# Optimization experiments

Measured on AMD Instinct MI355X. Metric: run time of the kernel, lower is better.

The kernel has to match this reference:

```python
import jax, jax.numpy as jnp
import numpy as np

V = 32000   # vocab_size
H = 512     # hidden_size
B = 16      # batch
T = 128     # target_len
S = 64      # encoder seq len
L = 1       # num_layers
BOS = 1     # vocab.bos_idx


def setup_inputs() -> dict:
    key = jax.random.key(0)
    ks = jax.random.split(key, 11)
    s = 0.02  # init scale
    return {
        "encoder_outputs": jax.random.normal(ks[0], (B, S, H), jnp.float32),
        "h0": jax.random.normal(ks[1], (L, B, H), jnp.float32) * 0.1,
        "c0": jax.random.normal(ks[2], (L, B, H), jnp.float32) * 0.1,
        "target_tensor": jax.random.randint(ks[3], (B, T), 0, V, dtype=jnp.int32).astype(jnp.int64),
        "emb": jax.random.normal(ks[4], (V, H), jnp.float32) * s,
        "W_ih": jax.random.normal(ks[5], (4 * H, H), jnp.float32) * s,
        "W_hh": jax.random.normal(ks[6], (4 * H, H), jnp.float32) * s,
        "b_ih": jnp.zeros((4 * H,), jnp.float32),
        "b_hh": jnp.zeros((4 * H,), jnp.float32),
        "W_out": jax.random.normal(ks[7], (V, H), jnp.float32) * s,
        "b_out": jnp.zeros((V,), jnp.float32),
    }


def reference(encoder_outputs, h0, c0, target_tensor, emb, W_ih, W_hh, b_ih, b_hh, W_out, b_out):
    # Teacher-forced input sequence: [BOS, target[:, :-1]]  -> [B, T]
    bsz = encoder_outputs.shape[0]
    bos = jnp.full((bsz, 1), BOS, dtype=target_tensor.dtype)
    toks = jnp.concatenate([bos, target_tensor[:, :-1]], axis=1)  # [B, T]

    h, c = h0[0], c0[0]  # num_layers == 1 -> [B, H]

    def step(carry, tok):
        h, c = carry
        x = jax.nn.relu(emb[tok])                               # embed + ReLU  [B, H]
        g = x @ W_ih.T + b_ih + h @ W_hh.T + b_hh               # [B, 4H], torch gate order i,f,g,o
        i, f, gg, o = jnp.split(g, 4, axis=-1)
        c2 = jax.nn.sigmoid(f) * c + jax.nn.sigmoid(i) * jnp.tanh(gg)
        h2 = jax.nn.sigmoid(o) * jnp.tanh(c2)
        logits = h2 @ W_out.T + b_out                           # [B, V]
        return (h2, c2), logits

    (hf, cf), logits = jax.lax.scan(step, (h, c), toks.T)       # scan over time
    decoder_outputs = logits.transpose(1, 0, 2)                 # [B, T, V]
    return decoder_outputs, hf[None], cf[None]
```

## Files before the change

### kernel.cpp

```cpp
#include <hip/hip_runtime.h>
#include <hip/hip_bf16.h>
#include <cstdint>


#define V_ 32000
#define H_ 512
#define B_ 16
#define T_ 128

typedef __attribute__((ext_vector_type(8))) short s16x8;
typedef __attribute__((ext_vector_type(4))) float f32x4;

typedef unsigned int __attribute__((address_space(1))) as1_u32;
typedef unsigned int __attribute__((address_space(3))) as3_u32;

__device__ __forceinline__ void async_cp16(const void* g, void* l) {
  __builtin_amdgcn_global_load_lds((const as1_u32*)g, (as3_u32*)l, 16, 0, 0);
}

__device__ __forceinline__ short f2bf(float f) {
  union { float f; unsigned u; } v; v.f = f;
  unsigned r = v.u + 0x7fffu + ((v.u >> 16) & 1u);
  return (short)(r >> 16);
}

__global__ void cvt_bf16(const float* __restrict__ in, short* __restrict__ out, int n4) {
  int i = blockIdx.x * blockDim.x + threadIdx.x;
  if (i >= n4) return;
  float4 v = ((const float4*)in)[i];
  short4 o;
  o.x = f2bf(v.x); o.y = f2bf(v.y); o.z = f2bf(v.z); o.w = f2bf(v.w);
  ((short4*)out)[i] = o;
}

__global__ void gather_embed(const float* __restrict__ emb, const int* __restrict__ tgt,
                             short* __restrict__ X, int* __restrict__ flags) {
  int m = blockIdx.x;
  int b = m >> 7, t = m & 127;
  int tok = (t == 0) ? 1 : tgt[b * T_ + t - 1];
  int k = threadIdx.x * 4;
  float4 v = *(const float4*)&emb[(size_t)tok * H_ + k];
  short4 o;
  o.x = f2bf(fmaxf(v.x, 0.f)); o.y = f2bf(fmaxf(v.y, 0.f));
  o.z = f2bf(fmaxf(v.z, 0.f)); o.w = f2bf(fmaxf(v.w, 0.f));
  *(short4*)&X[(size_t)m * H_ + k] = o;
  if (m == 0) flags[threadIdx.x] = 0;
}

__global__ __launch_bounds__(256, 2) void gemm_bt(
    const short* __restrict__ A, const short* __restrict__ B,
    const float* __restrict__ bias0, const float* __restrict__ bias1,
    float* __restrict__ out, int M, int N, int K, int ldo)
{
  __shared__ short As[1024 * 8];
  __shared__ short Bs[1024 * 8];
  const int tid = threadIdx.x;
  const int wave = tid >> 6, lane = tid & 63;
  const int row0 = blockIdx.y * 128, col0 = blockIdx.x * 128;
  const int m_in = lane & 15, quad = lane >> 4;
  const int wm = (wave >> 1) * 64, wn = (wave & 1) * 64;
  f32x4 acc[4][4] = {};
  for (int kt = 0; kt < K; kt += 64) {
    for (int i = 0; i < 4; ++i) {
      int s = (i * 4 + wave) * 64 + lane;
      int r = s >> 3, cs = s & 7, cd = cs ^ (r & 7);
      async_cp16(A + ((size_t)(row0 + r) * K + kt + cd * 8), &As[s * 8]);
      async_cp16(B + ((size_t)(col0 + r) * K + kt + cd * 8), &Bs[s * 8]);
    }
    __syncthreads();
    for (int kk = 0; kk < 2; ++kk) {
      s16x8 af[4], bfr[4];
      int c = kk * 4 + quad;
      for (int i = 0; i < 4; ++i) {
        int ra = wm + i * 16 + m_in;
        af[i] = *(const s16x8*)&As[(ra * 8 + (c ^ (ra & 7))) * 8];
        int rb = wn + i * 16 + m_in;
        bfr[i] = *(const s16x8*)&Bs[(rb * 8 + (c ^ (rb & 7))) * 8];
      }
      for (int i = 0; i < 4; ++i)
        for (int j = 0; j < 4; ++j)
          acc[i][j] = __builtin_amdgcn_mfma_f32_16x16x32_bf16(af[i], bfr[j], acc[i][j], 0, 0, 0);
    }
    __syncthreads();
  }
  for (int j = 0; j < 4; ++j) {
    int n = col0 + wn + j * 16 + m_in;
    float bs = bias0[n] + (bias1 ? bias1[n] : 0.f);
    for (int i = 0; i < 4; ++i) {
      int mrow = row0 + wm + i * 16 + quad * 4;
      f32x4 a = acc[i][j];
      for (int p = 0; p < 4; ++p)
        out[(size_t)(mrow + p) * ldo + n] = a[p] + bs;
    }
  }
}

__global__ __launch_bounds__(512, 1) void lstm_rec(
    const float* __restrict__ G0,
    const short* __restrict__ Whh,
    const float* __restrict__ h0, const float* __restrict__ c0,
    short* __restrict__ Hs,
    int* flags,
    float* __restrict__ hcf)
{
  __shared__ short Wl[8192 * 8];
  __shared__ short hl[1024 * 8];
  __shared__ float gl[128 * 17];

  const int S = blockIdx.x;
  const int tid = threadIdx.x, wave = tid >> 6, lane = tid & 63;
  const int nin = lane & 15, quad = lane >> 4;

  for (int i = tid; i < 8192; i += 512) {
    int r = i >> 6, cs = i & 63, cd = cs ^ (r & 7);
    int u = (r >> 5) * 512 + S * 32 + (r & 31);
    *(int4*)&Wl[i * 8] = *(const int4*)&Whh[(size_t)u * H_ + cd * 8];
  }
  const int batch = tid >> 5, hid = tid & 31;
  float c_reg = c0[batch * H_ + S * 32 + hid];
  __syncthreads();

  for (int tt = 0; tt < T_; ++tt) {
    if (tt > 0) {
      if (tid == 0) {
        while (__hip_atomic_load(&flags[tt - 1], __ATOMIC_RELAXED, __HIP_MEMORY_SCOPE_AGENT) < 16) {}
        __threadfence();
      }
      __syncthreads();
    }
    for (int i = tid; i < 1024; i += 512) {
      int m = i >> 6, cs = i & 63, cd = cs ^ (m & 7);
      if (tt == 0) {
        const float* hp = &h0[m * H_ + cd * 8];
        float4 v0 = *(const float4*)hp, v1 = *(const float4*)(hp + 4);
        s16x8 o;
        o[0] = f2bf(v0.x); o[1] = f2bf(v0.y); o[2] = f2bf(v0.z); o[3] = f2bf(v0.w);
        o[4] = f2bf(v1.x); o[5] = f2bf(v1.y); o[6] = f2bf(v1.z); o[7] = f2bf(v1.w);
        *(s16x8*)&hl[i * 8] = o;
      } else {
        *(int4*)&hl[i * 8] = *(const int4*)&Hs[((size_t)m * T_ + tt - 1) * H_ + cd * 8];
      }
    }
    __syncthreads();
    f32x4 acc = {};
    {
      int r = wave * 16 + nin;
      for (int ks = 0; ks < 16; ++ks) {
        int c = ks * 4 + quad;
        s16x8 af = *(const s16x8*)&hl[(nin * 64 + (c ^ (nin & 7))) * 8];
        s16x8 bf = *(const s16x8*)&Wl[(r * 64 + (c ^ (r & 7))) * 8];
        acc = __builtin_amdgcn_mfma_f32_16x16x32_bf16(af, bf, acc, 0, 0, 0);
      }
      int u = wave * 16 + nin;
      for (int p = 0; p < 4; ++p)
        gl[u * 17 + quad * 4 + p] = acc[p];
    }
    __syncthreads();
    {
      size_t gbase = ((size_t)batch * T_ + tt) * 2048 + S * 32 + hid;
      float xi = G0[gbase         ] + gl[(0 * 32 + hid) * 17 + batch];
      float xf = G0[gbase +  512  ] + gl[(1 * 32 + hid) * 17 + batch];
      float xg = G0[gbase + 1024  ] + gl[(2 * 32 + hid) * 17 + batch];
      float xo = G0[gbase + 1536  ] + gl[(3 * 32 + hid) * 17 + batch];
      float si = 1.f / (1.f + __expf(-xi));
      float sf = 1.f / (1.f + __expf(-xf));
      float so = 1.f / (1.f + __expf(-xo));
      c_reg = sf * c_reg + si * tanhf(xg);
      float hn = so * tanhf(c_reg);
      Hs[((size_t)batch * T_ + tt) * H_ + S * 32 + hid] = f2bf(hn);
      if (tt == T_ - 1) {
        hcf[(size_t)batch * H_ + S * 32 + hid] = hn;
        hcf[B_ * H_ + (size_t)batch * H_ + S * 32 + hid] = c_reg;
      }
    }
    __syncthreads();
    if (tid == 0) {
      __threadfence();
      __hip_atomic_fetch_add(&flags[tt], 1, __ATOMIC_RELAXED, __HIP_MEMORY_SCOPE_AGENT);
    }
  }
}

extern "C" void kernel_launch(void* const* d_in, const int* in_sizes, int n_in,
                              void* d_out, int out_size, void* d_ws, size_t ws_size,
                              hipStream_t stream) {
  (void)in_sizes; (void)n_in; (void)out_size; (void)ws_size;
  const float* h0   = (const float*)d_in[1];
  const float* c0   = (const float*)d_in[2];
  const int*   tgt  = (const int*)d_in[3];
  const float* emb  = (const float*)d_in[4];
  const float* Wih  = (const float*)d_in[5];
  const float* Whh  = (const float*)d_in[6];
  const float* bih  = (const float*)d_in[7];
  const float* bhh  = (const float*)d_in[8];
  const float* Wout = (const float*)d_in[9];
  const float* bout = (const float*)d_in[10];
  float* out = (float*)d_out;

  char* ws = (char*)d_ws;
  short* wsWout = (short*)(ws);
  short* wsWih  = (short*)(ws + 32768000);
  short* wsWhh  = (short*)(ws + 34865152);
  short* wsX    = (short*)(ws + 36962304);
  short* wsHs   = (short*)(ws + 39059456);
  int*   flags  = (int*)  (ws + 41156608);

  cvt_bf16<<<16000, 256, 0, stream>>>(Wout, wsWout, 4096000);
  cvt_bf16<<<1024, 256, 0, stream>>>(Wih, wsWih, 262144);
  cvt_bf16<<<1024, 256, 0, stream>>>(Whh, wsWhh, 262144);
  gather_embed<<<2048, 128, 0, stream>>>(emb, tgt, wsX, flags);
  gemm_bt<<<dim3(16, 16), 256, 0, stream>>>(wsX, wsWih, bih, bhh, out, 2048, 2048, 512, 2048);
  lstm_rec<<<16, 512, 0, stream>>>(out, wsWhh, h0, c0, wsHs, flags, out + (size_t)B_ * T_ * V_);
  gemm_bt<<<dim3(250, 16), 256, 0, stream>>>(wsHs, wsWout, bout, nullptr, out, 2048, 32000, 512, 32000);
}
```

Measured before the change: 947.5 us.

## Replace step-counter barrier with tagged double-buffered hidden-state exchange

The recurrent kernel no longer uses a global atomic counter plus threadfence per timestep. Each block now publishes its bf16 hidden values packed with a step tag into a double-buffered array (reusing the converted W_ih workspace). Consumers poll per element until the tag matches, so a block can proceed as soon as the data it needs has arrived, with no separate barrier round trip. The input-gate preactivations are loaded before the wait so their latency overlaps the polling. Separately, the GEMM grid axes are swapped so neighbouring blocks share the same weight column tile, which aims to improve cache reuse. The cost is more spinning atomic loads, and correctness relies on the tag bits never matching stale buffer contents.

Result: slower. 1.252 ms (+32.1%).

```diff
diff --git a/kernel.cpp b/kernel.cpp
--- a/kernel.cpp
+++ b/kernel.cpp
@@ -34,7 +34,7 @@
 }
 
 __global__ void gather_embed(const float* __restrict__ emb, const int* __restrict__ tgt,
-                             short* __restrict__ X, int* __restrict__ flags) {
+                             short* __restrict__ X) {
   int m = blockIdx.x;
   int b = m >> 7, t = m & 127;
   int tok = (t == 0) ? 1 : tgt[b * T_ + t - 1];
@@ -44,7 +44,6 @@
   o.x = f2bf(fmaxf(v.x, 0.f)); o.y = f2bf(fmaxf(v.y, 0.f));
   o.z = f2bf(fmaxf(v.z, 0.f)); o.w = f2bf(fmaxf(v.w, 0.f));
   *(short4*)&X[(size_t)m * H_ + k] = o;
-  if (m == 0) flags[threadIdx.x] = 0;
 }
 
 __global__ __launch_bounds__(256, 2) void gemm_bt(
@@ -56,7 +55,7 @@
   __shared__ short Bs[1024 * 8];
   const int tid = threadIdx.x;
   const int wave = tid >> 6, lane = tid & 63;
-  const int row0 = blockIdx.y * 128, col0 = blockIdx.x * 128;
+  const int row0 = blockIdx.x * 128, col0 = blockIdx.y * 128;
   const int m_in = lane & 15, quad = lane >> 4;
   const int wm = (wave >> 1) * 64, wn = (wave & 1) * 64;
   f32x4 acc[4][4] = {};
@@ -100,7 +99,7 @@
     const short* __restrict__ Whh,
     const float* __restrict__ h0, const float* __restrict__ c0,
     short* __restrict__ Hs,
-    int* flags,
+    unsigned* __restrict__ Hx,
     float* __restrict__ hcf)
 {
   __shared__ short Wl[8192 * 8];
@@ -121,29 +120,38 @@
   __syncthreads();
 
   for (int tt = 0; tt < T_; ++tt) {
-    if (tt > 0) {
-      if (tid == 0) {
-        while (__hip_atomic_load(&flags[tt - 1], __ATOMIC_RELAXED, __HIP_MEMORY_SCOPE_AGENT) < 16) {}
-        __threadfence();
-      }
-      __syncthreads();
-    }
-    for (int i = tid; i < 1024; i += 512) {
-      int m = i >> 6, cs = i & 63, cd = cs ^ (m & 7);
-      if (tt == 0) {
-        const float* hp = &h0[m * H_ + cd * 8];
-        float4 v0 = *(const float4*)hp, v1 = *(const float4*)(hp + 4);
-        s16x8 o;
-        o[0] = f2bf(v0.x); o[1] = f2bf(v0.y); o[2] = f2bf(v0.z); o[3] = f2bf(v0.w);
-        o[4] = f2bf(v1.x); o[5] = f2bf(v1.y); o[6] = f2bf(v1.z); o[7] = f2bf(v1.w);
-        *(s16x8*)&hl[i * 8] = o;
-      } else {
-        *(int4*)&hl[i * 8] = *(const int4*)&Hs[((size_t)m * T_ + tt - 1) * H_ + cd * 8];
-      }
-    }
-    __syncthreads();
-    f32x4 acc = {};
+    size_t gbase = ((size_t)batch * T_ + tt) * 2048 + S * 32 + hid;
+    float g0i = G0[gbase], g0f = G0[gbase + 512], g0g = G0[gbase + 1024], g0o = G0[gbase + 1536];
+
+    if (tt == 0) {
+      for (int j = 0; j < 16; ++j) {
+        short hv = f2bf(h0[j * H_ + tid]);
+        hl[(j * 64 + ((tid >> 3) ^ (j & 7))) * 8 + (tid & 7)] = hv;
+      }
+    } else {
+      const unsigned expect = (unsigned)tt;
+      unsigned* Hp = Hx + ((tt - 1) & 1) * (B_ * H_);
+      unsigned vals[16];
+      unsigned need = 0xFFFFu;
+      while (need) {
+        #pragma unroll
+        for (int j = 0; j < 16; ++j) {
+          if (need & (1u << j)) {
+            unsigned v = __hip_atomic_load(&Hp[j * H_ + tid], __ATOMIC_RELAXED,
+                                           __HIP_MEMORY_SCOPE_AGENT);
+            vals[j] = v;
+            if ((v >> 16) == expect) need &= ~(1u << j);
+          }
+        }
+      }
+      #pragma unroll
+      for (int j = 0; j < 16; ++j)
+        hl[(j * 64 + ((tid >> 3) ^ (j & 7))) * 8 + (tid & 7)] = (short)(vals[j] & 0xFFFFu);
+    }
+    __syncthreads();
+
     {
+      f32x4 acc = {};
       int r = wave * 16 + nin;
       for (int ks = 0; ks < 16; ++ks) {
         int c = ks * 4 + quad;
@@ -156,28 +164,28 @@
         gl[u * 17 + quad * 4 + p] = acc[p];
     }
     __syncthreads();
+
     {
-      size_t gbase = ((size_t)batch * T_ + tt) * 2048 + S * 32 + hid;
-      float xi = G0[gbase         ] + gl[(0 * 32 + hid) * 17 + batch];
-      float xf = G0[gbase +  512  ] + gl[(1 * 32 + hid) * 17 + batch];
-      float xg = G0[gbase + 1024  ] + gl[(2 * 32 + hid) * 17 + batch];
-      float xo = G0[gbase + 1536  ] + gl[(3 * 32 + hid) * 17 + batch];
+      float xi = g0i + gl[(0 * 32 + hid) * 17 + batch];
+      float xf = g0f + gl[(1 * 32 + hid) * 17 + batch];
+      float xg = g0g + gl[(2 * 32 + hid) * 17 + batch];
+      float xo = g0o + gl[(3 * 32 + hid) * 17 + batch];
       float si = 1.f / (1.f + __expf(-xi));
       float sf = 1.f / (1.f + __expf(-xf));
       float so = 1.f / (1.f + __expf(-xo));
       c_reg = sf * c_reg + si * tanhf(xg);
       float hn = so * tanhf(c_reg);
-      Hs[((size_t)batch * T_ + tt) * H_ + S * 32 + hid] = f2bf(hn);
+      short hb = f2bf(hn);
+      unsigned hv = ((unsigned)(tt + 1) << 16) | (unsigned short)hb;
+      __hip_atomic_store(&Hx[(tt & 1) * (B_ * H_) + batch * H_ + S * 32 + hid], hv,
+                         __ATOMIC_RELAXED, __HIP_MEMORY_SCOPE_AGENT);
+      Hs[((size_t)batch * T_ + tt) * H_ + S * 32 + hid] = hb;
       if (tt == T_ - 1) {
         hcf[(size_t)batch * H_ + S * 32 + hid] = hn;
         hcf[B_ * H_ + (size_t)batch * H_ + S * 32 + hid] = c_reg;
       }
     }
     __syncthreads();
-    if (tid == 0) {
-      __threadfence();
-      __hip_atomic_fetch_add(&flags[tt], 1, __ATOMIC_RELAXED, __HIP_MEMORY_SCOPE_AGENT);
-    }
   }
 }
 
@@ -203,13 +211,13 @@
   short* wsWhh  = (short*)(ws + 34865152);
   short* wsX    = (short*)(ws + 36962304);
   short* wsHs   = (short*)(ws + 39059456);
-  int*   flags  = (int*)  (ws + 41156608);
+  unsigned* Hx = (unsigned*)wsWih;
 
   cvt_bf16<<<16000, 256, 0, stream>>>(Wout, wsWout, 4096000);
   cvt_bf16<<<1024, 256, 0, stream>>>(Wih, wsWih, 262144);
   cvt_bf16<<<1024, 256, 0, stream>>>(Whh, wsWhh, 262144);
-  gather_embed<<<2048, 128, 0, stream>>>(emb, tgt, wsX, flags);
+  gather_embed<<<2048, 128, 0, stream>>>(emb, tgt, wsX);
   gemm_bt<<<dim3(16, 16), 256, 0, stream>>>(wsX, wsWih, bih, bhh, out, 2048, 2048, 512, 2048);
-  lstm_rec<<<16, 512, 0, stream>>>(out, wsWhh, h0, c0, wsHs, flags, out + (size_t)B_ * T_ * V_);
-  gemm_bt<<<dim3(250, 16), 256, 0, stream>>>(wsHs, wsWout, bout, nullptr, out, 2048, 32000, 512, 32000);
-}
+  lstm_rec<<<16, 512, 0, stream>>>(out, wsWhh, h0, c0, wsHs, Hx, out + (size_t)B_ * T_ * V_);
+  gemm_bt<<<dim3(16, 250), 256, 0, stream>>>(wsHs, wsWout, bout, nullptr, out, 2048, 32000, 512, 32000);
+}
```
